# Optimization experiments

Hardware: AMD Instinct MI355X
Metric: run time of the kernel (lower is better)

The kernel has to match this reference:

```python
import jax, jax.numpy as jnp
import numpy as np

BATCH, SEQ, D_MODEL, D_STATE = 8, 4096, 128, 128


def setup_inputs() -> dict:
    key = jax.random.key(0)
    ks = jax.random.split(key, 6)
    x = jax.random.normal(ks[0], (BATCH, SEQ, D_MODEL), jnp.float32)
    # Stable (negative) eigenvalues so A_discrete = exp(dt*Lambda) < 1 and powers don't overflow.
    Lam = -(jax.random.uniform(ks[1], (D_STATE,), jnp.float32) * 2.0 + 0.1)
    B = jax.random.normal(ks[2], (D_STATE, D_MODEL), jnp.float32) / np.sqrt(D_STATE)
    C = jax.random.normal(ks[3], (D_MODEL, D_STATE), jnp.float32) / np.sqrt(D_STATE)
    Dv = jax.random.normal(ks[4], (D_MODEL,), jnp.float32)
    log_dt = (jax.random.uniform(ks[5], (D_MODEL,), jnp.float32)
              * (np.log(0.001) - np.log(0.1)) + np.log(0.1)).astype(jnp.float32)
    return {"x": x, "Lam": Lam, "B": B, "C": C, "Dv": Dv, "log_dt": log_dt}


def _s4_forward(x, Lam, B, C, Dv, log_dt):
    # x: (batch, L, M) with transposed=False
    _, L, M = x.shape
    dt = jnp.exp(log_dt)                                    # (M,)
    rate = dt[:, None] * Lam[None, :]                       # (M, N) = log(A_discrete)
    ell = jnp.arange(L, dtype=x.dtype)                      # (L,)
    # powers[m, s, l] = A_discrete[m, s] ** l  (closed form of the sequential cumprod)
    powers = jnp.exp(rate[:, :, None] * ell[None, None, :])  # (M, N, L)
    # Original: einsum('ds,msl->dsl', B, powers) sums over m, giving B[d,s]*Psum[s,l];
    # then einsum('md,dsl->ml', C, .) contracts d and s -> kernel = C @ B @ Psum.
    Psum = powers.sum(axis=0)                               # (N, L)
    kernel = C @ (B @ Psum)                                 # (M, L)
    xt = jnp.transpose(x, (0, 2, 1))                        # (B, M, L)
    n = 2 * L  # zero-padded linear convolution via FFT
    y_fft = jnp.fft.rfft(xt, n=n) * jnp.fft.rfft(kernel, n=n)[None]
    y = jnp.fft.irfft(y_fft, n=n)[..., :L]                  # (B, M, L)
    y = y + Dv[None, :, None] * xt                          # skip connection D*u
    return jnp.transpose(y, (0, 2, 1))                      # (B, L, M)


def reference(x, Lam, B, C, Dv, log_dt):
    return _s4_forward(x, Lam, B, C, Dv, log_dt)
```

## Files before the change

kernel.cpp:

```cpp
#include <hip/hip_runtime.h>
#include <math.h>

#define BATCH 8
#define SEQ   4096
#define DM    128
#define DS    128
#define N2    4096
#define NT    256
#define NTP   256

__device__ __forceinline__ float2 cmulf(float2 a, float2 b) {
    return make_float2(a.x * b.x - a.y * b.y, a.x * b.y + a.y * b.x);
}
__device__ __forceinline__ float2 caddf(float2 a, float2 b) { return make_float2(a.x + b.x, a.y + b.y); }
__device__ __forceinline__ float2 csubf(float2 a, float2 b) { return make_float2(a.x - b.x, a.y - b.y); }
__device__ __forceinline__ float2 conjf2(float2 a) { return make_float2(a.x, -a.y); }
__device__ __forceinline__ float2 cisf(float t) { float s, c; __sincosf(t, &s, &c); return make_float2(c, s); }

__device__ __forceinline__ int nibrev(int k) { return ((k & 15) << 8) | (k & 0xF0) | (k >> 8); }
__device__ __forceinline__ int physi(int a) { return a ^ ((a >> 4) & 15); }

__device__ __forceinline__ void dft16_fwd(const float2 x[16], float2 Xh[16]) {
    const float2 W[10] = { {1.f,0.f},
        {0.92387953f,-0.38268343f},{0.70710678f,-0.70710678f},{0.38268343f,-0.92387953f},
        {0.f,-1.f},{-0.38268343f,-0.92387953f},{-0.70710678f,-0.70710678f},
        {-0.92387953f,-0.38268343f},{-1.f,0.f},{-0.92387953f,0.38268343f} };
    float2 y[16];
#pragma unroll
    for (int j = 0; j < 4; ++j) {
        float2 a0 = x[j], a1 = x[j+4], a2 = x[j+8], a3 = x[j+12];
        float2 t0 = caddf(a0,a2), t1 = csubf(a0,a2);
        float2 t2 = caddf(a1,a3), t3 = csubf(a1,a3);
        float2 b1 = make_float2(t1.x + t3.y, t1.y - t3.x);
        float2 b3 = make_float2(t1.x - t3.y, t1.y + t3.x);
        y[j]    = caddf(t0,t2);
        y[j+4]  = cmulf(b1, W[j]);
        y[j+8]  = cmulf(csubf(t0,t2), W[2*j]);
        y[j+12] = cmulf(b3, W[3*j]);
    }
#pragma unroll
    for (int g = 0; g < 4; ++g) {
        float2 a0 = y[4*g], a1 = y[4*g+1], a2 = y[4*g+2], a3 = y[4*g+3];
        float2 t0 = caddf(a0,a2), t1 = csubf(a0,a2);
        float2 t2 = caddf(a1,a3), t3 = csubf(a1,a3);
        Xh[4*g]   = caddf(t0,t2);
        Xh[4*g+1] = make_float2(t1.x + t3.y, t1.y - t3.x);
        Xh[4*g+2] = csubf(t0,t2);
        Xh[4*g+3] = make_float2(t1.x - t3.y, t1.y + t3.x);
    }
}
__device__ __forceinline__ void dft16_inv(const float2 x[16], float2 Xh[16]) {
    const float2 W[10] = { {1.f,0.f},
        {0.92387953f,0.38268343f},{0.70710678f,0.70710678f},{0.38268343f,0.92387953f},
        {0.f,1.f},{-0.38268343f,0.92387953f},{-0.70710678f,0.70710678f},
        {-0.92387953f,0.38268343f},{-1.f,0.f},{-0.92387953f,-0.38268343f} };
    float2 y[16];
#pragma unroll
    for (int j = 0; j < 4; ++j) {
        float2 a0 = x[j], a1 = x[j+4], a2 = x[j+8], a3 = x[j+12];
        float2 t0 = caddf(a0,a2), t1 = csubf(a0,a2);
        float2 t2 = caddf(a1,a3), t3 = csubf(a1,a3);
        float2 b1 = make_float2(t1.x - t3.y, t1.y + t3.x);
        float2 b3 = make_float2(t1.x + t3.y, t1.y - t3.x);
        y[j]    = caddf(t0,t2);
        y[j+4]  = cmulf(b1, W[j]);
        y[j+8]  = cmulf(csubf(t0,t2), W[2*j]);
        y[j+12] = cmulf(b3, W[3*j]);
    }
#pragma unroll
    for (int g = 0; g < 4; ++g) {
        float2 a0 = y[4*g], a1 = y[4*g+1], a2 = y[4*g+2], a3 = y[4*g+3];
        float2 t0 = caddf(a0,a2), t1 = csubf(a0,a2);
        float2 t2 = caddf(a1,a3), t3 = csubf(a1,a3);
        Xh[4*g]   = caddf(t0,t2);
        Xh[4*g+1] = make_float2(t1.x - t3.y, t1.y + t3.x);
        Xh[4*g+2] = csubf(t0,t2);
        Xh[4*g+3] = make_float2(t1.x + t3.y, t1.y - t3.x);
    }
}


template<int Q>
__device__ __forceinline__ void stage_fwd(float2* z, int t) {
    float2 x[16], Xh[16];
    int adr[16];
    if (Q == 16) {
        int j = t & 15, top = t >> 4;
#pragma unroll
        for (int r = 0; r < 16; ++r) adr[r] = (top << 8) + (r << 4) + (j ^ r);
    } else {
        int j4 = t & 15;
#pragma unroll
        for (int r = 0; r < 16; ++r) adr[r] = (t << 4) + (j4 ^ r);
    }
#pragma unroll
    for (int r = 0; r < 16; ++r) x[r] = z[adr[r]];
    dft16_fwd(x, Xh);
    if (Q > 1) {
        int j = t & (Q - 1);
        float2 w1 = cisf(-(float)M_PI / (8.0f * (float)Q) * (float)j);
        float2 w = make_float2(1.f, 0.f);
#pragma unroll
        for (int k = 0; k < 16; ++k) {
            int sk = ((k & 3) << 2) | (k >> 2);
            z[adr[k]] = cmulf(Xh[sk], w);
            w = cmulf(w, w1);
        }
    } else {
#pragma unroll
        for (int k = 0; k < 16; ++k) {
            int sk = ((k & 3) << 2) | (k >> 2);
            z[adr[k]] = Xh[sk];
        }
    }
}

template<int Q>
__device__ __forceinline__ void stage_inv(float2* z, int t) {
    float2 x[16], Xh[16];
    int adr[16];
    if (Q == 16) {
        int j = t & 15, top = t >> 4;
#pragma unroll
        for (int r = 0; r < 16; ++r) adr[r] = (top << 8) + (r << 4) + (j ^ r);
    } else {
        int j4 = t & 15;
#pragma unroll
        for (int r = 0; r < 16; ++r) adr[r] = (t << 4) + (j4 ^ r);
    }
    if (Q > 1) {
        int j = t & (Q - 1);
        float2 w1 = cisf((float)M_PI / (8.0f * (float)Q) * (float)j);
        float2 w = make_float2(1.f, 0.f);
#pragma unroll
        for (int k = 0; k < 16; ++k) {
            x[k] = cmulf(z[adr[k]], w);
            w = cmulf(w, w1);
        }
    } else {
#pragma unroll
        for (int k = 0; k < 16; ++k) x[k] = z[adr[k]];
    }
    dft16_inv(x, Xh);
#pragma unroll
    for (int r = 0; r < 16; ++r) {
        int sr = ((r & 3) << 2) | (r >> 2);
        z[adr[r]] = Xh[sr];
    }
}

__device__ __forceinline__ void fwd_first(float2* z, const float2* __restrict__ vrow, int t) {
    float2 x[16], Xh[16];
#pragma unroll
    for (int r = 0; r < 8; ++r) x[r] = vrow[t + (r << 8)];
#pragma unroll
    for (int r = 8; r < 16; ++r) x[r] = make_float2(0.f, 0.f);
    dft16_fwd(x, Xh);
    int b0 = t ^ ((t >> 4) & 15);
    float2 w1 = cisf(-(float)M_PI / 2048.0f * (float)t);
    float2 w = make_float2(1.f, 0.f);
#pragma unroll
    for (int k = 0; k < 16; ++k) {
        int sk = ((k & 3) << 2) | (k >> 2);
        z[b0 + (k << 8)] = cmulf(Xh[sk], w);
        w = cmulf(w, w1);
    }
}

__device__ __forceinline__ void inv_last_store(const float2* z, float2* __restrict__ xrow,
                                               int t, float dv) {
    float2 x[16], Xh[16];
    int b0 = t ^ ((t >> 4) & 15);
    float2 w1 = cisf((float)M_PI / 2048.0f * (float)t);
    float2 w = make_float2(1.f, 0.f);
#pragma unroll
    for (int k = 0; k < 16; ++k) {
        x[k] = cmulf(z[b0 + (k << 8)], w);
        w = cmulf(w, w1);
    }
    dft16_inv(x, Xh);
    const float invN = 1.0f / 4096.0f;
#pragma unroll
    for (int r = 0; r < 8; ++r) {
        int sr = ((r & 3) << 2) | (r >> 2);
        float2 res = Xh[sr];
        float2 xv = xrow[t + (r << 8)];
        xrow[t + (r << 8)] = make_float2(res.x * invN + dv * xv.x, res.y * invN + dv * xv.y);
    }
}


__global__ void prep_G(const float* __restrict__ Cm, const float* __restrict__ Bm,
                       float* __restrict__ GT) {
    int gid = blockIdx.x * blockDim.x + threadIdx.x;
    int m = gid >> 7, j = gid & 127;
    float acc = 0.f;
    for (int i = 0; i < DS; ++i) acc += Cm[m * DS + i] * Bm[i * DM + j];
    GT[j * DM + m] = acc;
}

__global__ void prep_psum2(const float* __restrict__ Lam, const float* __restrict__ logdt,
                           float* __restrict__ Psum) {
    __shared__ float E[DM];
    int s = blockIdx.x >> 1, half = blockIdx.x & 1;
    int t = threadIdx.x;
    if (t < DM) E[t] = __expf(logdt[t]) * Lam[s];
    __syncthreads();
    int l0 = t + 2048 * half;
    float acc[8] = {0.f,0.f,0.f,0.f,0.f,0.f,0.f,0.f};
    for (int m = 0; m < DM; ++m) {
        float e = E[m];
        float w = __expf(e * (float)l0);
        float r = __expf(e * 256.0f);
#pragma unroll
        for (int i = 0; i < 8; ++i) { acc[i] += w; w *= r; }
    }
#pragma unroll
    for (int i = 0; i < 8; ++i) Psum[s * SEQ + l0 + 256 * i] = acc[i];
}

__global__ void prep_K2(const float* __restrict__ GT, const float* __restrict__ Psum,
                        float* __restrict__ K) {
    __shared__ float4 PT[DS][4];
    int l0 = blockIdx.x * 16;
    int t = threadIdx.x;
    for (int idx = t; idx < 512; idx += NTP) {
        int s = idx >> 2, q = idx & 3;
        PT[s][q] = ((const float4*)(Psum + s * SEQ + l0))[q];
    }
    __syncthreads();
    int m = t & 127, half = t >> 7;
    float acc[8] = {0.f,0.f,0.f,0.f,0.f,0.f,0.f,0.f};
    for (int s = 0; s < DS; ++s) {
        float g = GT[s * DM + m];
        float4 p0 = PT[s][half * 2], p1 = PT[s][half * 2 + 1];
        acc[0] += g * p0.x; acc[1] += g * p0.y; acc[2] += g * p0.z; acc[3] += g * p0.w;
        acc[4] += g * p1.x; acc[5] += g * p1.y; acc[6] += g * p1.z; acc[7] += g * p1.w;
    }
    float4* kp = (float4*)(K + (size_t)m * SEQ + l0 + half * 8);
    kp[0] = make_float4(acc[0], acc[1], acc[2], acc[3]);
    kp[1] = make_float4(acc[4], acc[5], acc[6], acc[7]);
}

__device__ __forceinline__ void pq_one(float2 Kk, float2 Kkp, float thk,
                                       float2 fap, float2 fbp,
                                       float2* P, float2* Q) {
    float2 e  = cisf(-thk);
    float2 fa = make_float2(0.5f * (1.f + e.y), -0.5f * e.x);
    float2 fb = make_float2(0.5f * (1.f - e.y),  0.5f * e.x);
    float2 ak = cmulf(Kk, fa), bk = cmulf(Kk, fb);
    float2 apv = cmulf(Kkp, fap), bpv = cmulf(Kkp, fbp);
    float2 g = make_float2(0.5f * (1.f + e.y), 0.5f * e.x);
    float2 h = make_float2(0.5f * (1.f - e.y), -0.5f * e.x);
    *P = caddf(cmulf(g, ak), cmulf(h, conjf2(bpv)));
    *Q = caddf(cmulf(g, bk), cmulf(h, conjf2(apv)));
}
__device__ __forceinline__ void pq_pair(float2 Kk, float2 Kkp, float thk, float thkp,
                                        float2* Pk, float2* Qk, float2* Pkp, float2* Qkp) {
    float2 e  = cisf(-thk);
    float2 ep = cisf(-thkp);
    float2 fa  = make_float2(0.5f * (1.f + e.y),  -0.5f * e.x);
    float2 fb  = make_float2(0.5f * (1.f - e.y),   0.5f * e.x);
    float2 fap = make_float2(0.5f * (1.f + ep.y), -0.5f * ep.x);
    float2 fbp = make_float2(0.5f * (1.f - ep.y),  0.5f * ep.x);
    pq_one(Kk,  Kkp, thk,  fap, fbp, Pk,  Qk);
    pq_one(Kkp, Kk,  thkp, fa,  fb,  Pkp, Qkp);
}

__global__ void __launch_bounds__(NT, 4) fftK_PQ(const float* __restrict__ K,
                                                 float4* __restrict__ PQ) {
    __shared__ __align__(16) float2 z[N2];
    int t = threadIdx.x, m = blockIdx.x;
    const float2* krow = (const float2*)(K + (size_t)m * SEQ);

    fwd_first(z, krow, t);  __syncthreads();
    stage_fwd<16>(z, t);    __syncthreads();
    stage_fwd<1>(z, t);     __syncthreads();

    float4* dst = PQ + (size_t)m * 4096;
#pragma unroll
    for (int c = 0; c < 8; ++c) {
        int k = t + 256 * c;
        float2 Pk, Qk, Pkp, Qkp;
        if (k == 0) {
            float2 v0 = z[0];
            float2 v2 = z[8];
            float2 Ku0    = make_float2(v0.x + v0.y, 0.f);
            float2 Ku4096 = make_float2(v0.x - v0.y, 0.f);
            float2 Ku2048 = conjf2(v2);
            float2 Pd, Qd;
            pq_pair(Ku0, Ku4096, 0.f, (float)M_PI, &Pk, &Qk, &Pd, &Qd);
            float th2 = 0.5f * (float)M_PI;
            pq_pair(Ku2048, Ku2048, th2, th2, &Pkp, &Qkp, &Pd, &Qd);
        } else {
            int kp = 4096 - k;
            float2 va = z[physi(nibrev(k))];
            float2 vb = z[physi(nibrev(kp))];
            float thk  = (float)M_PI * (float)k / 4096.0f;
            float thkp = (float)M_PI - thk;
            float2 e  = cisf(-thk);
            float2 cb = conjf2(vb);
            float2 s  = caddf(va, cb), d = csubf(va, cb);
            float2 pr = cmulf(e, d);
            float2 Kuk = make_float2(0.5f * (s.x + pr.y), 0.5f * (s.y - pr.x));
            float2 ep = make_float2(-e.x, e.y);
            float2 ca = conjf2(va);
            float2 s2 = caddf(vb, ca), d2 = csubf(vb, ca);
            float2 p2 = cmulf(ep, d2);
            float2 Kukp = make_float2(0.5f * (s2.x + p2.y), 0.5f * (s2.y - p2.x));
            pq_pair(Kuk, Kukp, thk, thkp, &Pk, &Qk, &Pkp, &Qkp);
        }
        dst[2 * k]     = make_float4(Pk.x, Pk.y, Qk.x, Qk.y);
        dst[2 * k + 1] = make_float4(Pkp.x, Pkp.y, Qkp.x, Qkp.y);
    }
}

__global__ void transpose_xin(const float* __restrict__ x, float* __restrict__ xt) {
    __shared__ float tile[32][33];
    int b = blockIdx.z;
    int l0 = blockIdx.x * 32, m0 = blockIdx.y * 32;
    int tx = threadIdx.x, ty = threadIdx.y;
    for (int r = 0; r < 4; ++r) {
        int l = l0 + ty + r * 8;
        tile[ty + r * 8][tx] = x[(size_t)b * SEQ * DM + (size_t)l * DM + m0 + tx];
    }
    __syncthreads();
    for (int r = 0; r < 4; ++r) {
        int m = m0 + ty + r * 8;
        xt[(size_t)b * DM * SEQ + (size_t)m * SEQ + l0 + tx] = tile[tx][ty + r * 8];
    }
}
__global__ void transpose_yout(const float* __restrict__ yt, float* __restrict__ out) {
    __shared__ float tile[32][33];
    int b = blockIdx.z;
    int l0 = blockIdx.x * 32, m0 = blockIdx.y * 32;
    int tx = threadIdx.x, ty = threadIdx.y;
    for (int r = 0; r < 4; ++r) {
        int m = m0 + ty + r * 8;
        tile[ty + r * 8][tx] = yt[(size_t)b * DM * SEQ + (size_t)m * SEQ + l0 + tx];
    }
    __syncthreads();
    for (int r = 0; r < 4; ++r) {
        int l = l0 + ty + r * 8;
        out[(size_t)b * SEQ * DM + (size_t)l * DM + m0 + tx] = tile[tx][ty + r * 8];
    }
}

__global__ void __launch_bounds__(NT, 4) conv16(float* __restrict__ xt,
                                                const float4* __restrict__ PQ,
                                                const float* __restrict__ Dv) {
    __shared__ __align__(16) float2 z[N2];
    int t = threadIdx.x;
    int m = blockIdx.x & (DM - 1);
    int b = blockIdx.x >> 7;
    float2* xrow = (float2*)(xt + (((size_t)b * DM + m) << 12));

    fwd_first(z, xrow, t);  __syncthreads();
    stage_fwd<16>(z, t);    __syncthreads();
    stage_fwd<1>(z, t);     __syncthreads();

    {
        const float4* pq = PQ + (size_t)m * 4096;
#pragma unroll
        for (int c = 0; c < 8; ++c) {
            int k = t + 256 * c;
            float4 lo = pq[2 * k];
            float4 hi = pq[2 * k + 1];
            if (k == 0) {
                float2 v0 = z[0];
                z[0] = caddf(cmulf(make_float2(lo.x, lo.y), v0),
                             cmulf(make_float2(lo.z, lo.w), conjf2(v0)));
                float2 v2 = z[8];
                z[8] = caddf(cmulf(make_float2(hi.x, hi.y), v2),
                             cmulf(make_float2(hi.z, hi.w), conjf2(v2)));
            } else {
                int i  = physi(nibrev(k));
                int ip = physi(nibrev(4096 - k));
                float2 va = z[i], vb = z[ip];
                z[i]  = caddf(cmulf(make_float2(lo.x, lo.y), va),
                              cmulf(make_float2(lo.z, lo.w), conjf2(vb)));
                z[ip] = caddf(cmulf(make_float2(hi.x, hi.y), vb),
                              cmulf(make_float2(hi.z, hi.w), conjf2(va)));
            }
        }
    }
    __syncthreads();

    stage_inv<1>(z, t);     __syncthreads();
    stage_inv<16>(z, t);    __syncthreads();
    inv_last_store(z, xrow, t, Dv[m]);
}

extern "C" void kernel_launch(void* const* d_in, const int* in_sizes, int n_in,
                              void* d_out, int out_size, void* d_ws, size_t ws_size,
                              hipStream_t stream) {
    const float* x     = (const float*)d_in[0];
    const float* Lam   = (const float*)d_in[1];
    const float* Bm    = (const float*)d_in[2];
    const float* Cm    = (const float*)d_in[3];
    const float* Dv    = (const float*)d_in[4];
    const float* logdt = (const float*)d_in[5];
    float* out = (float*)d_out;

    float*  ws   = (float*)d_ws;
    float*  xt   = ws;
    float4* PQ   = (float4*)(ws + 4194304);
    float*  K    = ws + 4194304 + 2097152;
    float*  Psum = K + 524288;
    float*  GT   = Psum + 524288;

    hipLaunchKernelGGL(prep_G,         dim3(64),         dim3(NTP),    0, stream, Cm, Bm, GT);
    hipLaunchKernelGGL(prep_psum2,     dim3(256),        dim3(NTP),    0, stream, Lam, logdt, Psum);
    hipLaunchKernelGGL(prep_K2,        dim3(256),        dim3(NTP),    0, stream, GT, Psum, K);
    hipLaunchKernelGGL(fftK_PQ,        dim3(128),        dim3(NT),     0, stream, K, PQ);
    hipLaunchKernelGGL(transpose_xin,  dim3(128, 4, 8),  dim3(32, 8),  0, stream, x, xt);
    hipLaunchKernelGGL(conv16,         dim3(1024),       dim3(NT),     0, stream, xt, PQ, Dv);
    hipLaunchKernelGGL(transpose_yout, dim3(128, 4, 8),  dim3(32, 8),  0, stream, xt, out);
}
```

Baseline: 141.3 us.

## Switch FFT from radix-16 to radix-8 stages and fuse prep kernels

```diff
diff --git a/kernel.cpp b/kernel.cpp
--- a/kernel.cpp
+++ b/kernel.cpp
@@ -17,229 +17,107 @@
 __device__ __forceinline__ float2 conjf2(float2 a) { return make_float2(a.x, -a.y); }
 __device__ __forceinline__ float2 cisf(float t) { float s, c; __sincosf(t, &s, &c); return make_float2(c, s); }
 
-__device__ __forceinline__ int nibrev(int k) { return ((k & 15) << 8) | (k & 0xF0) | (k >> 8); }
+__device__ __forceinline__ int octrev(int k) {
+    return ((k & 7) << 9) | (((k >> 3) & 7) << 6) | (((k >> 6) & 7) << 3) | ((k >> 9) & 7);
+}
 __device__ __forceinline__ int physi(int a) { return a ^ ((a >> 4) & 15); }
 
-__device__ __forceinline__ void dft16_fwd(const float2 x[16], float2 Xh[16]) {
-    const float2 W[10] = { {1.f,0.f},
-        {0.92387953f,-0.38268343f},{0.70710678f,-0.70710678f},{0.38268343f,-0.92387953f},
-        {0.f,-1.f},{-0.38268343f,-0.92387953f},{-0.70710678f,-0.70710678f},
-        {-0.92387953f,-0.38268343f},{-1.f,0.f},{-0.92387953f,0.38268343f} };
-    float2 y[16];
-#pragma unroll
-    for (int j = 0; j < 4; ++j) {
-        float2 a0 = x[j], a1 = x[j+4], a2 = x[j+8], a3 = x[j+12];
-        float2 t0 = caddf(a0,a2), t1 = csubf(a0,a2);
-        float2 t2 = caddf(a1,a3), t3 = csubf(a1,a3);
-        float2 b1 = make_float2(t1.x + t3.y, t1.y - t3.x);
-        float2 b3 = make_float2(t1.x - t3.y, t1.y + t3.x);
-        y[j]    = caddf(t0,t2);
-        y[j+4]  = cmulf(b1, W[j]);
-        y[j+8]  = cmulf(csubf(t0,t2), W[2*j]);
-        y[j+12] = cmulf(b3, W[3*j]);
-    }
-#pragma unroll
-    for (int g = 0; g < 4; ++g) {
-        float2 a0 = y[4*g], a1 = y[4*g+1], a2 = y[4*g+2], a3 = y[4*g+3];
-        float2 t0 = caddf(a0,a2), t1 = csubf(a0,a2);
-        float2 t2 = caddf(a1,a3), t3 = csubf(a1,a3);
-        Xh[4*g]   = caddf(t0,t2);
-        Xh[4*g+1] = make_float2(t1.x + t3.y, t1.y - t3.x);
-        Xh[4*g+2] = csubf(t0,t2);
-        Xh[4*g+3] = make_float2(t1.x - t3.y, t1.y + t3.x);
-    }
-}
-__device__ __forceinline__ void dft16_inv(const float2 x[16], float2 Xh[16]) {
-    const float2 W[10] = { {1.f,0.f},
-        {0.92387953f,0.38268343f},{0.70710678f,0.70710678f},{0.38268343f,0.92387953f},
-        {0.f,1.f},{-0.38268343f,0.92387953f},{-0.70710678f,0.70710678f},
-        {-0.92387953f,0.38268343f},{-1.f,0.f},{-0.92387953f,-0.38268343f} };
-    float2 y[16];
-#pragma unroll
-    for (int j = 0; j < 4; ++j) {
-        float2 a0 = x[j], a1 = x[j+4], a2 = x[j+8], a3 = x[j+12];
-        float2 t0 = caddf(a0,a2), t1 = csubf(a0,a2);
-        float2 t2 = caddf(a1,a3), t3 = csubf(a1,a3);
-        float2 b1 = make_float2(t1.x - t3.y, t1.y + t3.x);
-        float2 b3 = make_float2(t1.x + t3.y, t1.y - t3.x);
-        y[j]    = caddf(t0,t2);
-        y[j+4]  = cmulf(b1, W[j]);
-        y[j+8]  = cmulf(csubf(t0,t2), W[2*j]);
-        y[j+12] = cmulf(b3, W[3*j]);
-    }
-#pragma unroll
-    for (int g = 0; g < 4; ++g) {
-        float2 a0 = y[4*g], a1 = y[4*g+1], a2 = y[4*g+2], a3 = y[4*g+3];
-        float2 t0 = caddf(a0,a2), t1 = csubf(a0,a2);
-        float2 t2 = caddf(a1,a3), t3 = csubf(a1,a3);
-        Xh[4*g]   = caddf(t0,t2);
-        Xh[4*g+1] = make_float2(t1.x - t3.y, t1.y + t3.x);
-        Xh[4*g+2] = csubf(t0,t2);
-        Xh[4*g+3] = make_float2(t1.x + t3.y, t1.y - t3.x);
-    }
-}
-
+#define RC8 0.70710678f
+__device__ __forceinline__ void dft8_fwd(const float2 x[8], float2 X[8]) {
+    float2 t0=caddf(x[0],x[4]), t1=caddf(x[1],x[5]), t2=caddf(x[2],x[6]), t3=caddf(x[3],x[7]);
+    float2 d0=csubf(x[0],x[4]), d1=csubf(x[1],x[5]), d2=csubf(x[2],x[6]), d3=csubf(x[3],x[7]);
+    float2 u0=d0;
+    float2 u1=make_float2(RC8*(d1.x+d1.y), RC8*(d1.y-d1.x));
+    float2 u2=make_float2(d2.y, -d2.x);
+    float2 u3=make_float2(RC8*(d3.y-d3.x), -RC8*(d3.x+d3.y));
+    float2 s0=caddf(t0,t2), s1=csubf(t0,t2), s2=caddf(t1,t3), s3=csubf(t1,t3);
+    float2 s3m=make_float2(s3.y,-s3.x);
+    X[0]=caddf(s0,s2); X[4]=csubf(s0,s2); X[2]=caddf(s1,s3m); X[6]=csubf(s1,s3m);
+    float2 q0=caddf(u0,u2), q1=csubf(u0,u2), q2=caddf(u1,u3), q3=csubf(u1,u3);
+    float2 q3m=make_float2(q3.y,-q3.x);
+    X[1]=caddf(q0,q2); X[5]=csubf(q0,q2); X[3]=caddf(q1,q3m); X[7]=csubf(q1,q3m);
+}
+__device__ __forceinline__ void dft8_inv(const float2 x[8], float2 X[8]) {
+    float2 t0=caddf(x[0],x[4]), t1=caddf(x[1],x[5]), t2=caddf(x[2],x[6]), t3=caddf(x[3],x[7]);
+    float2 d0=csubf(x[0],x[4]), d1=csubf(x[1],x[5]), d2=csubf(x[2],x[6]), d3=csubf(x[3],x[7]);
+    float2 u0=d0;
+    float2 u1=make_float2(RC8*(d1.x-d1.y), RC8*(d1.x+d1.y));
+    float2 u2=make_float2(-d2.y, d2.x);
+    float2 u3=make_float2(-RC8*(d3.x+d3.y), RC8*(d3.x-d3.y));
+    float2 s0=caddf(t0,t2), s1=csubf(t0,t2), s2=caddf(t1,t3), s3=csubf(t1,t3);
+    float2 s3p=make_float2(-s3.y,s3.x);
+    X[0]=caddf(s0,s2); X[4]=csubf(s0,s2); X[2]=caddf(s1,s3p); X[6]=csubf(s1,s3p);
+    float2 q0=caddf(u0,u2), q1=csubf(u0,u2), q2=caddf(u1,u3), q3=csubf(u1,u3);
+    float2 q3p=make_float2(-q3.y,q3.x);
+    X[1]=caddf(q0,q2); X[5]=csubf(q0,q2); X[3]=caddf(q1,q3p); X[7]=csubf(q1,q3p);
+}
+
+#define TW_CHAIN(w1) \
+    float2 w2 = cmulf(w1, w1); float2 w4 = cmulf(w2, w2); float2 w3 = cmulf(w2, w1); \
+    float2 w5 = cmulf(w4, w1); float2 w6 = cmulf(w4, w2); float2 w7 = cmulf(w4, w3);
 
 template<int Q>
-__device__ __forceinline__ void stage_fwd(float2* z, int t) {
-    float2 x[16], Xh[16];
-    int adr[16];
-    if (Q == 16) {
-        int j = t & 15, top = t >> 4;
-#pragma unroll
-        for (int r = 0; r < 16; ++r) adr[r] = (top << 8) + (r << 4) + (j ^ r);
-    } else {
-        int j4 = t & 15;
-#pragma unroll
-        for (int r = 0; r < 16; ++r) adr[r] = (t << 4) + (j4 ^ r);
-    }
-#pragma unroll
-    for (int r = 0; r < 16; ++r) x[r] = z[adr[r]];
-    dft16_fwd(x, Xh);
-    if (Q > 1) {
-        int j = t & (Q - 1);
-        float2 w1 = cisf(-(float)M_PI / (8.0f * (float)Q) * (float)j);
-        float2 w = make_float2(1.f, 0.f);
-#pragma unroll
-        for (int k = 0; k < 16; ++k) {
-            int sk = ((k & 3) << 2) | (k >> 2);
-            z[adr[k]] = cmulf(Xh[sk], w);
-            w = cmulf(w, w1);
-        }
-    } else {
-#pragma unroll
-        for (int k = 0; k < 16; ++k) {
-            int sk = ((k & 3) << 2) | (k >> 2);
-            z[adr[k]] = Xh[sk];
-        }
-    }
-}
-
+__device__ __forceinline__ void stage8_fwd(float2* z, int t) {
+#pragma unroll
+    for (int h = 0; h < 2; ++h) {
+        int idx = t + 256 * h;
+        int j = idx & (Q - 1);
+        int base = ((idx & ~(Q - 1)) << 3) | j;
+        int adr[8];
+        float2 x[8], X[8];
+#pragma unroll
+        for (int r = 0; r < 8; ++r) { adr[r] = physi(base + Q * r); x[r] = z[adr[r]]; }
+        dft8_fwd(x, X);
+        if (Q > 1) {
+            float2 w1 = cisf(-(float)M_PI / (4.0f * (float)Q) * (float)j);
+            TW_CHAIN(w1);
+            X[1]=cmulf(X[1],w1); X[2]=cmulf(X[2],w2); X[3]=cmulf(X[3],w3); X[4]=cmulf(X[4],w4);
+            X[5]=cmulf(X[5],w5); X[6]=cmulf(X[6],w6); X[7]=cmulf(X[7],w7);
+        }
+#pragma unroll
+        for (int r = 0; r < 8; ++r) z[adr[r]] = X[r];
+    }
+}
 template<int Q>
-__device__ __forceinline__ void stage_inv(float2* z, int t) {
-    float2 x[16], Xh[16];
-    int adr[16];
-    if (Q == 16) {
-        int j = t & 15, top = t >> 4;
-#pragma unroll
-        for (int r = 0; r < 16; ++r) adr[r] = (top << 8) + (r << 4) + (j ^ r);
-    } else {
-        int j4 = t & 15;
-#pragma unroll
-        for (int r = 0; r < 16; ++r) adr[r] = (t << 4) + (j4 ^ r);
-    }
-    if (Q > 1) {
-        int j = t & (Q - 1);
-        float2 w1 = cisf((float)M_PI / (8.0f * (float)Q) * (float)j);
-        float2 w = make_float2(1.f, 0.f);
-#pragma unroll
-        for (int k = 0; k < 16; ++k) {
-            x[k] = cmulf(z[adr[k]], w);
-            w = cmulf(w, w1);
-        }
-    } else {
-#pragma unroll
-        for (int k = 0; k < 16; ++k) x[k] = z[adr[k]];
-    }
-    dft16_inv(x, Xh);
-#pragma unroll
-    for (int r = 0; r < 16; ++r) {
-        int sr = ((r & 3) << 2) | (r >> 2);
-        z[adr[r]] = Xh[sr];
-    }
-}
-
-__device__ __forceinline__ void fwd_first(float2* z, const float2* __restrict__ vrow, int t) {
-    float2 x[16], Xh[16];
-#pragma unroll
-    for (int r = 0; r < 8; ++r) x[r] = vrow[t + (r << 8)];
-#pragma unroll
-    for (int r = 8; r < 16; ++r) x[r] = make_float2(0.f, 0.f);
-    dft16_fwd(x, Xh);
-    int b0 = t ^ ((t >> 4) & 15);
-    float2 w1 = cisf(-(float)M_PI / 2048.0f * (float)t);
-    float2 w = make_float2(1.f, 0.f);
-#pragma unroll
-    for (int k = 0; k < 16; ++k) {
-        int sk = ((k & 3) << 2) | (k >> 2);
-        z[b0 + (k << 8)] = cmulf(Xh[sk], w);
-        w = cmulf(w, w1);
-    }
-}
-
-__device__ __forceinline__ void inv_last_store(const float2* z, float2* __restrict__ xrow,
-                                               int t, float dv) {
-    float2 x[16], Xh[16];
-    int b0 = t ^ ((t >> 4) & 15);
-    float2 w1 = cisf((float)M_PI / 2048.0f * (float)t);
-    float2 w = make_float2(1.f, 0.f);
-#pragma unroll
-    for (int k = 0; k < 16; ++k) {
-        x[k] = cmulf(z[b0 + (k << 8)], w);
-        w = cmulf(w, w1);
-    }
-    dft16_inv(x, Xh);
-    const float invN = 1.0f / 4096.0f;
-#pragma unroll
-    for (int r = 0; r < 8; ++r) {
-        int sr = ((r & 3) << 2) | (r >> 2);
-        float2 res = Xh[sr];
-        float2 xv = xrow[t + (r << 8)];
-        xrow[t + (r << 8)] = make_float2(res.x * invN + dv * xv.x, res.y * invN + dv * xv.y);
-    }
-}
-
-
-__global__ void prep_G(const float* __restrict__ Cm, const float* __restrict__ Bm,
-                       float* __restrict__ GT) {
-    int gid = blockIdx.x * blockDim.x + threadIdx.x;
-    int m = gid >> 7, j = gid & 127;
-    float acc = 0.f;
-    for (int i = 0; i < DS; ++i) acc += Cm[m * DS + i] * Bm[i * DM + j];
-    GT[j * DM + m] = acc;
-}
-
-__global__ void prep_psum2(const float* __restrict__ Lam, const float* __restrict__ logdt,
-                           float* __restrict__ Psum) {
-    __shared__ float E[DM];
-    int s = blockIdx.x >> 1, half = blockIdx.x & 1;
-    int t = threadIdx.x;
-    if (t < DM) E[t] = __expf(logdt[t]) * Lam[s];
-    __syncthreads();
-    int l0 = t + 2048 * half;
-    float acc[8] = {0.f,0.f,0.f,0.f,0.f,0.f,0.f,0.f};
-    for (int m = 0; m < DM; ++m) {
-        float e = E[m];
-        float w = __expf(e * (float)l0);
-        float r = __expf(e * 256.0f);
-#pragma unroll
-        for (int i = 0; i < 8; ++i) { acc[i] += w; w *= r; }
-    }
-#pragma unroll
-    for (int i = 0; i < 8; ++i) Psum[s * SEQ + l0 + 256 * i] = acc[i];
-}
-
-__global__ void prep_K2(const float* __restrict__ GT, const float* __restrict__ Psum,
-                        float* __restrict__ K) {
-    __shared__ float4 PT[DS][4];
-    int l0 = blockIdx.x * 16;
-    int t = threadIdx.x;
-    for (int idx = t; idx < 512; idx += NTP) {
-        int s = idx >> 2, q = idx & 3;
-        PT[s][q] = ((const float4*)(Psum + s * SEQ + l0))[q];
-    }
-    __syncthreads();
-    int m = t & 127, half = t >> 7;
-    float acc[8] = {0.f,0.f,0.f,0.f,0.f,0.f,0.f,0.f};
-    for (int s = 0; s < DS; ++s) {
-        float g = GT[s * DM + m];
-        float4 p0 = PT[s][half * 2], p1 = PT[s][half * 2 + 1];
-        acc[0] += g * p0.x; acc[1] += g * p0.y; acc[2] += g * p0.z; acc[3] += g * p0.w;
-        acc[4] += g * p1.x; acc[5] += g * p1.y; acc[6] += g * p1.z; acc[7] += g * p1.w;
-    }
-    float4* kp = (float4*)(K + (size_t)m * SEQ + l0 + half * 8);
-    kp[0] = make_float4(acc[0], acc[1], acc[2], acc[3]);
-    kp[1] = make_float4(acc[4], acc[5], acc[6], acc[7]);
+__device__ __forceinline__ void stage8_inv(float2* z, int t) {
+#pragma unroll
+    for (int h = 0; h < 2; ++h) {
+        int idx = t + 256 * h;
+        int j = idx & (Q - 1);
+        int base = ((idx & ~(Q - 1)) << 3) | j;
+        int adr[8];
+        float2 x[8], X[8];
+#pragma unroll
+        for (int r = 0; r < 8; ++r) { adr[r] = physi(base + Q * r); x[r] = z[adr[r]]; }
+        if (Q > 1) {
+            float2 w1 = cisf((float)M_PI / (4.0f * (float)Q) * (float)j);
+            TW_CHAIN(w1);
+            x[1]=cmulf(x[1],w1); x[2]=cmulf(x[2],w2); x[3]=cmulf(x[3],w3); x[4]=cmulf(x[4],w4);
+            x[5]=cmulf(x[5],w5); x[6]=cmulf(x[6],w6); x[7]=cmulf(x[7],w7);
+        }
+        dft8_inv(x, X);
+#pragma unroll
+        for (int r = 0; r < 8; ++r) z[adr[r]] = X[r];
+    }
+}
+
+__device__ __forceinline__ void fwd_first8(float2* z, const float2* __restrict__ vrow, int t) {
+#pragma unroll
+    for (int h = 0; h < 2; ++h) {
+        int idx = t + 256 * h;
+        float2 x[8], X[8];
+#pragma unroll
+        for (int r = 0; r < 4; ++r) x[r] = vrow[idx + 512 * r];
+#pragma unroll
+        for (int r = 4; r < 8; ++r) x[r] = make_float2(0.f, 0.f);
+        dft8_fwd(x, X);
+        float2 w1 = cisf(-(float)M_PI / 2048.0f * (float)idx);
+        TW_CHAIN(w1);
+        X[1]=cmulf(X[1],w1); X[2]=cmulf(X[2],w2); X[3]=cmulf(X[3],w3); X[4]=cmulf(X[4],w4);
+        X[5]=cmulf(X[5],w5); X[6]=cmulf(X[6],w6); X[7]=cmulf(X[7],w7);
+#pragma unroll
+        for (int r = 0; r < 8; ++r) z[physi(idx + 512 * r)] = X[r];
+    }
 }
 
 __device__ __forceinline__ void pq_one(float2 Kk, float2 Kkp, float thk,
@@ -267,24 +145,95 @@
     pq_one(Kkp, Kk,  thkp, fa,  fb,  Pkp, Qkp);
 }
 
+__global__ void __launch_bounds__(NTP) prep_fused(
+    const float* __restrict__ x, float* __restrict__ xt,
+    const float* __restrict__ Lam, const float* __restrict__ logdt, float* __restrict__ Psum,
+    const float* __restrict__ Cm, const float* __restrict__ Bm, float* __restrict__ GT) {
+    int bid = blockIdx.x, t = threadIdx.x;
+    if (bid < 4096) {
+        __shared__ float tile[32][33];
+        int l0 = (bid & 127) * 32, m0 = ((bid >> 7) & 3) * 32, b = bid >> 9;
+        int tx = t & 31, ty = t >> 5;
+#pragma unroll
+        for (int r = 0; r < 4; ++r) {
+            int l = l0 + ty + r * 8;
+            tile[ty + r * 8][tx] = x[(size_t)b * SEQ * DM + (size_t)l * DM + m0 + tx];
+        }
+        __syncthreads();
+#pragma unroll
+        for (int r = 0; r < 4; ++r) {
+            int m = m0 + ty + r * 8;
+            xt[(size_t)b * DM * SEQ + (size_t)m * SEQ + l0 + tx] = tile[tx][ty + r * 8];
+        }
+    } else if (bid < 4352) {
+        __shared__ float E[DM];
+        int sb = bid - 4096;
+        int s = sb >> 1, half = sb & 1;
+        if (t < DM) E[t] = __expf(logdt[t]) * Lam[s];
+        __syncthreads();
+        int l0 = t + 2048 * half;
+        float acc[8] = {0.f,0.f,0.f,0.f,0.f,0.f,0.f,0.f};
+        for (int m = 0; m < DM; ++m) {
+            float e = E[m];
+            float w = __expf(e * (float)l0);
+            float r = __expf(e * 256.0f);
+#pragma unroll
+            for (int i = 0; i < 8; ++i) { acc[i] += w; w *= r; }
+        }
+#pragma unroll
+        for (int i = 0; i < 8; ++i) Psum[s * SEQ + l0 + 256 * i] = acc[i];
+    } else {
+        int gid = (bid - 4352) * NTP + t;
+        int m = gid >> 7, j = gid & 127;
+        float acc = 0.f;
+        for (int i = 0; i < DS; ++i) acc += Cm[m * DS + i] * Bm[i * DM + j];
+        GT[j * DM + m] = acc;
+    }
+}
+
+__global__ void prep_K2(const float* __restrict__ GT, const float* __restrict__ Psum,
+                        float* __restrict__ K) {
+    __shared__ float4 PT[DS][4];
+    int l0 = blockIdx.x * 16;
+    int t = threadIdx.x;
+    for (int idx = t; idx < 512; idx += NTP) {
+        int s = idx >> 2, q = idx & 3;
+        PT[s][q] = ((const float4*)(Psum + s * SEQ + l0))[q];
+    }
+    __syncthreads();
+    int m = t & 127, half = t >> 7;
+    float acc[8] = {0.f,0.f,0.f,0.f,0.f,0.f,0.f,0.f};
+    for (int s = 0; s < DS; ++s) {
+        float g = GT[s * DM + m];
+        float4 p0 = PT[s][half * 2], p1 = PT[s][half * 2 + 1];
+        acc[0] += g * p0.x; acc[1] += g * p0.y; acc[2] += g * p0.z; acc[3] += g * p0.w;
+        acc[4] += g * p1.x; acc[5] += g * p1.y; acc[6] += g * p1.z; acc[7] += g * p1.w;
+    }
+    float4* kp = (float4*)(K + (size_t)m * SEQ + l0 + half * 8);
+    kp[0] = make_float4(acc[0], acc[1], acc[2], acc[3]);
+    kp[1] = make_float4(acc[4], acc[5], acc[6], acc[7]);
+}
+
 __global__ void __launch_bounds__(NT, 4) fftK_PQ(const float* __restrict__ K,
                                                  float4* __restrict__ PQ) {
     __shared__ __align__(16) float2 z[N2];
     int t = threadIdx.x, m = blockIdx.x;
     const float2* krow = (const float2*)(K + (size_t)m * SEQ);
 
-    fwd_first(z, krow, t);  __syncthreads();
-    stage_fwd<16>(z, t);    __syncthreads();
-    stage_fwd<1>(z, t);     __syncthreads();
+    fwd_first8(z, krow, t); __syncthreads();
+    stage8_fwd<64>(z, t);   __syncthreads();
+    stage8_fwd<8>(z, t);    __syncthreads();
+    stage8_fwd<1>(z, t);    __syncthreads();
 
     float4* dst = PQ + (size_t)m * 4096;
 #pragma unroll
     for (int c = 0; c < 8; ++c) {
-        int k = t + 256 * c;
+        int slot = (c << 8) | t;
+        int k = (t << 3) | c;
         float2 Pk, Qk, Pkp, Qkp;
         if (k == 0) {
             float2 v0 = z[0];
-            float2 v2 = z[8];
+            float2 v2 = z[4];
             float2 Ku0    = make_float2(v0.x + v0.y, 0.f);
             float2 Ku4096 = make_float2(v0.x - v0.y, 0.f);
             float2 Ku2048 = conjf2(v2);
@@ -294,8 +243,8 @@
             pq_pair(Ku2048, Ku2048, th2, th2, &Pkp, &Qkp, &Pd, &Qd);
         } else {
             int kp = 4096 - k;
-            float2 va = z[physi(nibrev(k))];
-            float2 vb = z[physi(nibrev(kp))];
+            float2 va = z[physi(octrev(k))];
+            float2 vb = z[physi(octrev(kp))];
             float thk  = (float)M_PI * (float)k / 4096.0f;
             float thkp = (float)M_PI - thk;
             float2 e  = cisf(-thk);
@@ -310,72 +259,43 @@
             float2 Kukp = make_float2(0.5f * (s2.x + p2.y), 0.5f * (s2.y - p2.x));
             pq_pair(Kuk, Kukp, thk, thkp, &Pk, &Qk, &Pkp, &Qkp);
         }
-        dst[2 * k]     = make_float4(Pk.x, Pk.y, Qk.x, Qk.y);
-        dst[2 * k + 1] = make_float4(Pkp.x, Pkp.y, Qkp.x, Qkp.y);
-    }
-}
-
-__global__ void transpose_xin(const float* __restrict__ x, float* __restrict__ xt) {
-    __shared__ float tile[32][33];
-    int b = blockIdx.z;
-    int l0 = blockIdx.x * 32, m0 = blockIdx.y * 32;
-    int tx = threadIdx.x, ty = threadIdx.y;
-    for (int r = 0; r < 4; ++r) {
-        int l = l0 + ty + r * 8;
-        tile[ty + r * 8][tx] = x[(size_t)b * SEQ * DM + (size_t)l * DM + m0 + tx];
-    }
-    __syncthreads();
-    for (int r = 0; r < 4; ++r) {
-        int m = m0 + ty + r * 8;
-        xt[(size_t)b * DM * SEQ + (size_t)m * SEQ + l0 + tx] = tile[tx][ty + r * 8];
-    }
-}
-__global__ void transpose_yout(const float* __restrict__ yt, float* __restrict__ out) {
-    __shared__ float tile[32][33];
-    int b = blockIdx.z;
-    int l0 = blockIdx.x * 32, m0 = blockIdx.y * 32;
-    int tx = threadIdx.x, ty = threadIdx.y;
-    for (int r = 0; r < 4; ++r) {
-        int m = m0 + ty + r * 8;
-        tile[ty + r * 8][tx] = yt[(size_t)b * DM * SEQ + (size_t)m * SEQ + l0 + tx];
-    }
-    __syncthreads();
-    for (int r = 0; r < 4; ++r) {
-        int l = l0 + ty + r * 8;
-        out[(size_t)b * SEQ * DM + (size_t)l * DM + m0 + tx] = tile[tx][ty + r * 8];
-    }
-}
-
-__global__ void __launch_bounds__(NT, 4) conv16(float* __restrict__ xt,
-                                                const float4* __restrict__ PQ,
-                                                const float* __restrict__ Dv) {
+        dst[2 * slot]     = make_float4(Pk.x, Pk.y, Qk.x, Qk.y);
+        dst[2 * slot + 1] = make_float4(Pkp.x, Pkp.y, Qkp.x, Qkp.y);
+    }
+}
+
+__global__ void __launch_bounds__(NT, 4) conv8(float* __restrict__ xt,
+                                               const float4* __restrict__ PQ,
+                                               const float* __restrict__ Dv) {
     __shared__ __align__(16) float2 z[N2];
     int t = threadIdx.x;
     int m = blockIdx.x & (DM - 1);
     int b = blockIdx.x >> 7;
     float2* xrow = (float2*)(xt + (((size_t)b * DM + m) << 12));
 
-    fwd_first(z, xrow, t);  __syncthreads();
-    stage_fwd<16>(z, t);    __syncthreads();
-    stage_fwd<1>(z, t);     __syncthreads();
+    fwd_first8(z, xrow, t); __syncthreads();
+    stage8_fwd<64>(z, t);   __syncthreads();
+    stage8_fwd<8>(z, t);    __syncthreads();
+    stage8_fwd<1>(z, t);    __syncthreads();
 
     {
         const float4* pq = PQ + (size_t)m * 4096;
 #pragma unroll
         for (int c = 0; c < 8; ++c) {
-            int k = t + 256 * c;
-            float4 lo = pq[2 * k];
-            float4 hi = pq[2 * k + 1];
+            int slot = (c << 8) | t;
+            int k = (t << 3) | c;
+            float4 lo = pq[2 * slot];
+            float4 hi = pq[2 * slot + 1];
             if (k == 0) {
                 float2 v0 = z[0];
                 z[0] = caddf(cmulf(make_float2(lo.x, lo.y), v0),
                              cmulf(make_float2(lo.z, lo.w), conjf2(v0)));
-                float2 v2 = z[8];
-                z[8] = caddf(cmulf(make_float2(hi.x, hi.y), v2),
+                float2 v2 = z[4];
+                z[4] = caddf(cmulf(make_float2(hi.x, hi.y), v2),
                              cmulf(make_float2(hi.z, hi.w), conjf2(v2)));
             } else {
-                int i  = physi(nibrev(k));
-                int ip = physi(nibrev(4096 - k));
+                int i  = physi(octrev(k));
+                int ip = physi(octrev(4096 - k));
                 float2 va = z[i], vb = z[ip];
                 z[i]  = caddf(cmulf(make_float2(lo.x, lo.y), va),
                               cmulf(make_float2(lo.z, lo.w), conjf2(vb)));
@@ -386,9 +306,54 @@
     }
     __syncthreads();
 
-    stage_inv<1>(z, t);     __syncthreads();
-    stage_inv<16>(z, t);    __syncthreads();
-    inv_last_store(z, xrow, t, Dv[m]);
+    stage8_inv<1>(z, t);    __syncthreads();
+    stage8_inv<8>(z, t);    __syncthreads();
+    stage8_inv<64>(z, t);   __syncthreads();
+
+    {
+        const float invN = 1.0f / 4096.0f;
+        float dv = Dv[m];
+#pragma unroll
+        for (int h = 0; h < 2; ++h) {
+            int idx = t + 256 * h;
+            float2 y[8], D[8];
+            float2 w1 = cisf((float)M_PI / 2048.0f * (float)idx);
+            TW_CHAIN(w1);
+            y[0] = z[physi(idx)];
+            y[1] = cmulf(z[physi(idx + 512)],  w1);
+            y[2] = cmulf(z[physi(idx + 1024)], w2);
+            y[3] = cmulf(z[physi(idx + 1536)], w3);
+            y[4] = cmulf(z[physi(idx + 2048)], w4);
+            y[5] = cmulf(z[physi(idx + 2560)], w5);
+            y[6] = cmulf(z[physi(idx + 3072)], w6);
+            y[7] = cmulf(z[physi(idx + 3584)], w7);
+            dft8_inv(y, D);
+#pragma unroll
+            for (int r = 0; r < 4; ++r) {
+                int n = idx + 512 * r;
+                float2 xv = xrow[n];
+                xrow[n] = make_float2(D[r].x * invN + dv * xv.x, D[r].y * invN + dv * xv.y);
+            }
+        }
+    }
+}
+
+__global__ void transpose_yout(const float* __restrict__ yt, float* __restrict__ out) {
+    __shared__ float tile[32][33];
+    int b = blockIdx.z;
+    int l0 = blockIdx.x * 32, m0 = blockIdx.y * 32;
+    int tx = threadIdx.x, ty = threadIdx.y;
+#pragma unroll
+    for (int r = 0; r < 4; ++r) {
+        int m = m0 + ty + r * 8;
+        tile[ty + r * 8][tx] = yt[(size_t)b * DM * SEQ + (size_t)m * SEQ + l0 + tx];
+    }
+    __syncthreads();
+#pragma unroll
+    for (int r = 0; r < 4; ++r) {
+        int l = l0 + ty + r * 8;
+        out[(size_t)b * SEQ * DM + (size_t)l * DM + m0 + tx] = tile[tx][ty + r * 8];
+    }
 }
 
 extern "C" void kernel_launch(void* const* d_in, const int* in_sizes, int n_in,
@@ -409,11 +374,10 @@
     float*  Psum = K + 524288;
     float*  GT   = Psum + 524288;
 
-    hipLaunchKernelGGL(prep_G,         dim3(64),         dim3(NTP),    0, stream, Cm, Bm, GT);
-    hipLaunchKernelGGL(prep_psum2,     dim3(256),        dim3(NTP),    0, stream, Lam, logdt, Psum);
+    hipLaunchKernelGGL(prep_fused,     dim3(4416),       dim3(NTP),    0, stream,
+                       x, xt, Lam, logdt, Psum, Cm, Bm, GT);
     hipLaunchKernelGGL(prep_K2,        dim3(256),        dim3(NTP),    0, stream, GT, Psum, K);
     hipLaunchKernelGGL(fftK_PQ,        dim3(128),        dim3(NT),     0, stream, K, PQ);
-    hipLaunchKernelGGL(transpose_xin,  dim3(128, 4, 8),  dim3(32, 8),  0, stream, x, xt);
-    hipLaunchKernelGGL(conv16,         dim3(1024),       dim3(NT),     0, stream, xt, PQ, Dv);
+    hipLaunchKernelGGL(conv8,          dim3(1024),       dim3(NT),     0, stream, xt, PQ, Dv);
     hipLaunchKernelGGL(transpose_yout, dim3(128, 4, 8),  dim3(32, 8),  0, stream, xt, out);
 }
```

After: 149.3 us. 1.06x slower.
